# Kernel tuning notes

Measured on AMD Instinct MI355X. Metric: run time of the kernel, lower is better.

## Reference

```python
import jax, jax.numpy as jnp
import numpy as np

DIM = 1024
H = 16
HD = 64

def setup_inputs() -> dict:
    key = jax.random.key(0)
    ks = jax.random.split(key, 5)
    x = jax.random.normal(ks[0], (2, 2048, DIM), dtype=jnp.float32)
    gamma = jnp.ones((DIM,), jnp.float32)
    beta = jnp.zeros((DIM,), jnp.float32)
    w_qkv = jax.random.normal(ks[1], (DIM, 3 * H * HD), dtype=jnp.float32) * (DIM ** -0.5)
    w_out = jax.random.normal(ks[2], (H * HD, DIM), dtype=jnp.float32) * ((H * HD) ** -0.5)
    b_out = jnp.zeros((DIM,), jnp.float32)
    return {"x": x, "gamma": gamma, "beta": beta, "w_qkv": w_qkv, "w_out": w_out, "b_out": b_out}

def reference(x, gamma, beta, w_qkv, w_out, b_out):
    # LayerNorm (pre-norm)
    mu = jnp.mean(x, axis=-1, keepdims=True)
    var = jnp.var(x, axis=-1, keepdims=True)
    xn = (x - mu) * jax.lax.rsqrt(var + 1e-5) * gamma + beta
    # QKV projection (no bias)
    qkv = xn @ w_qkv  # (b, n, 3*h*hd)
    q, k, v = jnp.split(qkv, 3, axis=-1)
    b, n, _ = x.shape
    split = lambda t: t.reshape(b, n, H, HD).transpose(0, 2, 1, 3)  # b h n d
    q, k, v = split(q), split(k), split(v)
    scale = HD ** -0.5
    scores = jnp.einsum('bhqd,bhkd->bhqk', q, k) * scale
    weights = jax.nn.softmax(scores, axis=-1)
    attn = jnp.einsum('bhqk,bhkd->bhqd', weights, v)  # b h n d
    attn = attn.transpose(0, 2, 1, 3).reshape(b, n, H * HD)
    # output projection (dropout is identity in eval)
    return attn @ w_out + b_out
```

## Files before the change

### kernel.cpp

```cpp
#include <hip/hip_runtime.h>
#include <hip/hip_bf16.h>


typedef _Float16 f16x8 __attribute__((ext_vector_type(8)));
typedef _Float16 f16x4 __attribute__((ext_vector_type(4)));
typedef float    f32x4 __attribute__((ext_vector_type(4)));

#define DIM   1024
#define NH    16
#define HD2   64
#define SEQ   2048
#define ROWS  4096
#define QKVN  3072

__device__ __forceinline__ void async_copy16(void* lds, const void* gsrc) {
    __builtin_amdgcn_global_load_lds(
        (const __attribute__((address_space(1))) unsigned int*)gsrc,
        (__attribute__((address_space(3))) unsigned int*)lds, 16, 0, 0);
}

__global__ __launch_bounds__(256) void ln_kernel(
    const float* __restrict__ x, const float* __restrict__ gamma,
    const float* __restrict__ beta, _Float16* __restrict__ xn) {
    const int row = blockIdx.x;
    const int t = threadIdx.x;
    const float4 v = reinterpret_cast<const float4*>(x + (size_t)row * DIM)[t];
    float s1 = v.x + v.y + v.z + v.w;
    float s2 = v.x * v.x + v.y * v.y + v.z * v.z + v.w * v.w;
    for (int off = 32; off; off >>= 1) {
        s1 += __shfl_down(s1, off);
        s2 += __shfl_down(s2, off);
    }
    __shared__ float red[8];
    const int wv = t >> 6, lane = t & 63;
    if (lane == 0) { red[wv * 2] = s1; red[wv * 2 + 1] = s2; }
    __syncthreads();
    s1 = red[0] + red[2] + red[4] + red[6];
    s2 = red[1] + red[3] + red[5] + red[7];
    const float mu = s1 * (1.0f / DIM);
    const float var = s2 * (1.0f / DIM) - mu * mu;
    const float rstd = rsqrtf(var + 1e-5f);
    const float4 g = reinterpret_cast<const float4*>(gamma)[t];
    const float4 bb = reinterpret_cast<const float4*>(beta)[t];
    f16x4 o;
    o[0] = (_Float16)((v.x - mu) * rstd * g.x + bb.x);
    o[1] = (_Float16)((v.y - mu) * rstd * g.y + bb.y);
    o[2] = (_Float16)((v.z - mu) * rstd * g.z + bb.z);
    o[3] = (_Float16)((v.w - mu) * rstd * g.w + bb.w);
    reinterpret_cast<f16x4*>(xn + (size_t)row * DIM)[t] = o;
}

__global__ __launch_bounds__(256) void transpose_cvt_kernel(
    const float* __restrict__ in, _Float16* __restrict__ out, int R, int C) {
    __shared__ float tile[32][33];
    const int c0 = blockIdx.x * 32, r0 = blockIdx.y * 32;
    const int tx = threadIdx.x, ty = threadIdx.y;
#pragma unroll
    for (int i = 0; i < 4; i++)
        tile[ty + i * 8][tx] = in[(size_t)(r0 + ty + i * 8) * C + c0 + tx];
    __syncthreads();
#pragma unroll
    for (int i = 0; i < 4; i++)
        out[(size_t)(c0 + ty + i * 8) * R + r0 + tx] = (_Float16)tile[tx][ty + i * 8];
}

__global__ __launch_bounds__(256) void gemm_qkv_kernel(
    const _Float16* __restrict__ A, const _Float16* __restrict__ Bt,
    _Float16* __restrict__ qk, _Float16* __restrict__ vT, int K) {
    __shared__ _Float16 Al[2][128 * 32];
    __shared__ _Float16 Bl[2][128 * 32];
    const int t = threadIdx.x, wv = t >> 6, lane = t & 63;
    const int lg = lane >> 4, lr = lane & 15;
    const int wr = wv >> 1, wc = wv & 1;
    const int m0 = blockIdx.y * 128, n0 = blockIdx.x * 128;

    f32x4 acc[4][4] = {};

    const int srow = t >> 2, sk = (t & 3) * 8;
    const _Float16* Ag0 = A + (size_t)(m0 + srow) * K + sk;
    const _Float16* Bg0 = Bt + (size_t)(n0 + srow) * K + sk;

    auto STAGE = [&](int buf, int k0) {
        _Float16* Alw = &Al[buf][wv * 512];
        _Float16* Blw = &Bl[buf][wv * 512];
        async_copy16(Alw,        Ag0 + k0);
        async_copy16(Alw + 2048, Ag0 + (size_t)64 * K + k0);
        async_copy16(Blw,        Bg0 + k0);
        async_copy16(Blw + 2048, Bg0 + (size_t)64 * K + k0);
    };

    STAGE(0, 0);
    asm volatile("s_waitcnt vmcnt(0)" ::: "memory");
    __builtin_amdgcn_s_barrier();
    int cur = 0;
    for (int k0 = 0; k0 < K; k0 += 32) {
        if (k0 + 32 < K) STAGE(cur ^ 1, k0 + 32);
        const _Float16* Ab = &Al[cur][0];
        const _Float16* Bb = &Bl[cur][0];
        f16x8 af[4], bfr[4];
#pragma unroll
        for (int m = 0; m < 4; m++)
            af[m] = *reinterpret_cast<const f16x8*>(&Ab[(wr * 64 + m * 16 + lr) * 32 + lg * 8]);
#pragma unroll
        for (int n = 0; n < 4; n++)
            bfr[n] = *reinterpret_cast<const f16x8*>(&Bb[(wc * 64 + n * 16 + lr) * 32 + lg * 8]);
#pragma unroll
        for (int m = 0; m < 4; m++)
#pragma unroll
            for (int n = 0; n < 4; n++)
                acc[m][n] = __builtin_amdgcn_mfma_f32_16x16x32_f16(af[m], bfr[n], acc[m][n], 0, 0, 0);
        asm volatile("s_waitcnt vmcnt(0)" ::: "memory");
        __builtin_amdgcn_s_barrier();
        cur ^= 1;
    }

    if (n0 < 2 * DIM) {
#pragma unroll
        for (int m = 0; m < 4; m++) {
            const int row = m0 + wr * 64 + m * 16 + lg * 4;
#pragma unroll
            for (int n = 0; n < 4; n++) {
                const int col = n0 + wc * 64 + n * 16 + lr;
#pragma unroll
                for (int jj = 0; jj < 4; jj++)
                    qk[(size_t)(row + jj) * 2048 + col] = (_Float16)acc[m][n][jj];
            }
        }
    } else {
#pragma unroll
        for (int m = 0; m < 4; m++) {
            const int row = m0 + wr * 64 + m * 16 + lg * 4;
            const int b = row >> 11, nn = row & 2047;
#pragma unroll
            for (int n = 0; n < 4; n++) {
                const int vcol = n0 + wc * 64 + n * 16 + lr - 2 * DIM;
                f16x4 pk;
#pragma unroll
                for (int jj = 0; jj < 4; jj++) pk[jj] = (_Float16)acc[m][n][jj];
                *reinterpret_cast<f16x4*>(&vT[(size_t)(b * 1024 + vcol) * SEQ + nn]) = pk;
            }
        }
    }
}

__global__ __launch_bounds__(256) void gemm_out_kernel(
    const _Float16* __restrict__ A, const _Float16* __restrict__ Bt,
    float* __restrict__ C, const float* __restrict__ bias, int N, int K) {
    __shared__ _Float16 Al[2][128 * 32];
    __shared__ _Float16 Bl[2][64 * 32];
    const int t = threadIdx.x, wv = t >> 6, lane = t & 63;
    const int lg = lane >> 4, lr = lane & 15;
    const int wr = wv >> 1, wc = wv & 1;
    const int m0 = blockIdx.y * 128, n0 = blockIdx.x * 64;

    f32x4 acc[4][2] = {};

    const int srow = t >> 2, sk = (t & 3) * 8;
    const _Float16* Ag0 = A + (size_t)(m0 + srow) * K + sk;
    const _Float16* Bg0 = Bt + (size_t)(n0 + srow) * K + sk;

    auto STAGE = [&](int buf, int k0) {
        _Float16* Alw = &Al[buf][wv * 512];
        _Float16* Blw = &Bl[buf][wv * 512];
        async_copy16(Alw,        Ag0 + k0);
        async_copy16(Alw + 2048, Ag0 + (size_t)64 * K + k0);
        async_copy16(Blw,        Bg0 + k0);
    };

    STAGE(0, 0);
    asm volatile("s_waitcnt vmcnt(0)" ::: "memory");
    __builtin_amdgcn_s_barrier();
    int cur = 0;
    for (int k0 = 0; k0 < K; k0 += 32) {
        if (k0 + 32 < K) STAGE(cur ^ 1, k0 + 32);
        const _Float16* Ab = &Al[cur][0];
        const _Float16* Bb = &Bl[cur][0];
        f16x8 af[4], bfr[2];
#pragma unroll
        for (int m = 0; m < 4; m++)
            af[m] = *reinterpret_cast<const f16x8*>(&Ab[(wr * 64 + m * 16 + lr) * 32 + lg * 8]);
#pragma unroll
        for (int n = 0; n < 2; n++)
            bfr[n] = *reinterpret_cast<const f16x8*>(&Bb[(wc * 32 + n * 16 + lr) * 32 + lg * 8]);
#pragma unroll
        for (int m = 0; m < 4; m++)
#pragma unroll
            for (int n = 0; n < 2; n++)
                acc[m][n] = __builtin_amdgcn_mfma_f32_16x16x32_f16(af[m], bfr[n], acc[m][n], 0, 0, 0);
        asm volatile("s_waitcnt vmcnt(0)" ::: "memory");
        __builtin_amdgcn_s_barrier();
        cur ^= 1;
    }

#pragma unroll
    for (int m = 0; m < 4; m++) {
        const int row = m0 + wr * 64 + m * 16 + lg * 4;
#pragma unroll
        for (int n = 0; n < 2; n++) {
            const int col = n0 + wc * 32 + n * 16 + lr;
            const float bo = bias[col];
#pragma unroll
            for (int jj = 0; jj < 4; jj++)
                C[(size_t)(row + jj) * N + col] = acc[m][n][jj] + bo;
        }
    }
}

__global__ __launch_bounds__(256) void attn_fa_kernel(
    const _Float16* __restrict__ qk, const _Float16* __restrict__ vT,
    _Float16* __restrict__ attn) {
    const int id = blockIdx.x;
    const int nid = (id & 7) * 128 + (id >> 3);
    const int bh = nid >> 5, b = bh >> 4, h = bh & 15;
    const int q0 = (nid & 31) * 64;
    const int t = threadIdx.x, wv = t >> 6, lane = t & 63;
    const int lg = lane >> 4, lr = lane & 15;

    __shared__ _Float16 Kl[64][72];
    __shared__ _Float16 Vt[64][72];
    __shared__ _Float16 PT[4][16][72];

    const size_t qrow = (size_t)(b * SEQ + q0 + wv * 16 + lr);
    const _Float16* qp = qk + qrow * 2048 + h * HD2;
    f16x8 qf0 = *reinterpret_cast<const f16x8*>(qp + lg * 8);
    f16x8 qf1 = *reinterpret_cast<const f16x8*>(qp + 32 + lg * 8);
    qf0 = qf0 * (_Float16)0.125f;
    qf1 = qf1 * (_Float16)0.125f;

    f32x4 o[4] = {};
    float mrun = -INFINITY, lrun = 0.f;

    const int sr = t >> 3, sc = (t & 7) * 8;
    const _Float16* kbase = qk + (size_t)(b * SEQ + sr) * 2048 + DIM + h * HD2 + sc;
    const _Float16* vbase = vT + (size_t)(bh * HD2 + sr) * SEQ + sc;

    f16x8 rk0 = *reinterpret_cast<const f16x8*>(kbase);
    f16x8 rk1 = *reinterpret_cast<const f16x8*>(kbase + (size_t)32 * 2048);
    f16x8 rv0 = *reinterpret_cast<const f16x8*>(vbase);
    f16x8 rv1 = *reinterpret_cast<const f16x8*>(vbase + (size_t)32 * SEQ);

    for (int kv0 = 0; kv0 < SEQ; kv0 += 64) {
        __builtin_amdgcn_s_barrier();
        *reinterpret_cast<f16x8*>(&Kl[sr][sc])      = rk0;
        *reinterpret_cast<f16x8*>(&Kl[sr + 32][sc]) = rk1;
        *reinterpret_cast<f16x8*>(&Vt[sr][sc])      = rv0;
        *reinterpret_cast<f16x8*>(&Vt[sr + 32][sc]) = rv1;
        if (kv0 + 64 < SEQ) {
            const _Float16* kp = kbase + (size_t)(kv0 + 64) * 2048;
            const _Float16* vp = vbase + (kv0 + 64);
            rk0 = *reinterpret_cast<const f16x8*>(kp);
            rk1 = *reinterpret_cast<const f16x8*>(kp + (size_t)32 * 2048);
            rv0 = *reinterpret_cast<const f16x8*>(vp);
            rv1 = *reinterpret_cast<const f16x8*>(vp + (size_t)32 * SEQ);
        }
        asm volatile("s_waitcnt lgkmcnt(0)" ::: "memory");
        __builtin_amdgcn_s_barrier();

        f32x4 s[4];
#pragma unroll
        for (int n = 0; n < 4; n++) {
            f16x8 kf0 = *reinterpret_cast<const f16x8*>(&Kl[n * 16 + lr][lg * 8]);
            f16x8 kf1 = *reinterpret_cast<const f16x8*>(&Kl[n * 16 + lr][32 + lg * 8]);
            f32x4 z = {0.f, 0.f, 0.f, 0.f};
            __builtin_amdgcn_s_setprio(1);
            z = __builtin_amdgcn_mfma_f32_16x16x32_f16(kf0, qf0, z, 0, 0, 0);
            z = __builtin_amdgcn_mfma_f32_16x16x32_f16(kf1, qf1, z, 0, 0, 0);
            __builtin_amdgcn_s_setprio(0);
            s[n] = z;
        }

        float m1 = fmaxf(fmaxf(s[0][0], s[0][1]), fmaxf(s[0][2], s[0][3]));
#pragma unroll
        for (int n = 1; n < 4; n++)
            m1 = fmaxf(m1, fmaxf(fmaxf(s[n][0], s[n][1]), fmaxf(s[n][2], s[n][3])));
        m1 = fmaxf(m1, __shfl_xor(m1, 16));
        m1 = fmaxf(m1, __shfl_xor(m1, 32));
        if (!__all(m1 - mrun <= 8.f)) {
            const float mnew = fmaxf(mrun, m1);
            const float corr = __expf(mrun - mnew);
            mrun = mnew;
            lrun *= corr;
#pragma unroll
            for (int dn = 0; dn < 4; dn++) o[dn] *= corr;
        }
        float rsum = 0.f;
#pragma unroll
        for (int n = 0; n < 4; n++)
#pragma unroll
            for (int jj = 0; jj < 4; jj++) {
                const float p = __expf(s[n][jj] - mrun);
                s[n][jj] = p;
                rsum += p;
            }
        rsum += __shfl_xor(rsum, 16);
        rsum += __shfl_xor(rsum, 32);
        lrun += rsum;

#pragma unroll
        for (int n = 0; n < 4; n++) {
            f16x4 pk;
#pragma unroll
            for (int jj = 0; jj < 4; jj++) pk[jj] = (_Float16)s[n][jj];
            *reinterpret_cast<f16x4*>(&PT[wv][lr][n * 16 + lg * 4]) = pk;
        }
        f16x8 pa0 = *reinterpret_cast<const f16x8*>(&PT[wv][lr][lg * 8]);
        f16x8 pa1 = *reinterpret_cast<const f16x8*>(&PT[wv][lr][32 + lg * 8]);

#pragma unroll
        for (int dn = 0; dn < 4; dn++) {
            f16x8 vf0 = *reinterpret_cast<const f16x8*>(&Vt[dn * 16 + lr][lg * 8]);
            f16x8 vf1 = *reinterpret_cast<const f16x8*>(&Vt[dn * 16 + lr][32 + lg * 8]);
            __builtin_amdgcn_s_setprio(1);
            o[dn] = __builtin_amdgcn_mfma_f32_16x16x32_f16(vf0, pa0, o[dn], 0, 0, 0);
            o[dn] = __builtin_amdgcn_mfma_f32_16x16x32_f16(vf1, pa1, o[dn], 0, 0, 0);
            __builtin_amdgcn_s_setprio(0);
        }
    }

    const float inv = 1.0f / lrun;
    const size_t orow = (size_t)(b * SEQ + q0 + wv * 16 + lr);
#pragma unroll
    for (int dn = 0; dn < 4; dn++) {
        f16x4 pk;
#pragma unroll
        for (int jj = 0; jj < 4; jj++) pk[jj] = (_Float16)(o[dn][jj] * inv);
        *reinterpret_cast<f16x4*>(&attn[orow * DIM + h * HD2 + dn * 16 + lg * 4]) = pk;
    }
}

extern "C" void kernel_launch(void* const* d_in, const int* in_sizes, int n_in,
                              void* d_out, int out_size, void* d_ws, size_t ws_size,
                              hipStream_t stream) {
    const float* x     = (const float*)d_in[0];
    const float* gamma = (const float*)d_in[1];
    const float* beta  = (const float*)d_in[2];
    const float* w_qkv = (const float*)d_in[3];
    const float* w_out = (const float*)d_in[4];
    const float* b_out = (const float*)d_in[5];
    float* out = (float*)d_out;

    _Float16* ws    = (_Float16*)d_ws;
    _Float16* xn    = ws;
    _Float16* wqkvT = xn + (size_t)ROWS * DIM;
    _Float16* woutT = wqkvT + (size_t)QKVN * DIM;
    _Float16* qk    = woutT + (size_t)DIM * DIM;
    _Float16* vT    = qk + (size_t)ROWS * 2048;
    _Float16* attnb = xn;

    ln_kernel<<<ROWS, 256, 0, stream>>>(x, gamma, beta, xn);
    transpose_cvt_kernel<<<dim3(QKVN / 32, DIM / 32), dim3(32, 8), 0, stream>>>(w_qkv, wqkvT, DIM, QKVN);
    transpose_cvt_kernel<<<dim3(DIM / 32, DIM / 32), dim3(32, 8), 0, stream>>>(w_out, woutT, DIM, DIM);
    gemm_qkv_kernel<<<dim3(QKVN / 128, ROWS / 128), 256, 0, stream>>>(xn, wqkvT, qk, vT, DIM);
    attn_fa_kernel<<<1024, 256, 0, stream>>>(qk, vT, attnb);
    gemm_out_kernel<<<dim3(DIM / 64, ROWS / 128), 256, 0, stream>>>(attnb, woutT, out, b_out, DIM, DIM);
}
```

Measured before the change: 217.2 us.

## Load K/V fragments directly from global memory, dropping LDS staging and barriers

The attention kernel no longer stages K and V tiles in shared memory with register prefetch and block barriers. Each wave now reads its MFMA operand fragments for K and V straight from global memory every iteration. This removes the LDS writes, LDS reads and two barriers per tile. In exchange, the four waves in a block each fetch the same K/V data (4x redundant global/L2 traffic), and the software prefetch is lost, so load latency sits exposed right before the MFMAs.

```diff
diff --git a/kernel.cpp b/kernel.cpp
--- a/kernel.cpp
+++ b/kernel.cpp
@@ -216,8 +216,6 @@
     const int t = threadIdx.x, wv = t >> 6, lane = t & 63;
     const int lg = lane >> 4, lr = lane & 15;
 
-    __shared__ _Float16 Kl[64][72];
-    __shared__ _Float16 Vt[64][72];
     __shared__ _Float16 PT[4][16][72];
 
     const size_t qrow = (size_t)(b * SEQ + q0 + wv * 16 + lr);
@@ -230,41 +228,31 @@
     f32x4 o[4] = {};
     float mrun = -INFINITY, lrun = 0.f;
 
-    const int sr = t >> 3, sc = (t & 7) * 8;
-    const _Float16* kbase = qk + (size_t)(b * SEQ + sr) * 2048 + DIM + h * HD2 + sc;
-    const _Float16* vbase = vT + (size_t)(bh * HD2 + sr) * SEQ + sc;
-
-    f16x8 rk0 = *reinterpret_cast<const f16x8*>(kbase);
-    f16x8 rk1 = *reinterpret_cast<const f16x8*>(kbase + (size_t)32 * 2048);
-    f16x8 rv0 = *reinterpret_cast<const f16x8*>(vbase);
-    f16x8 rv1 = *reinterpret_cast<const f16x8*>(vbase + (size_t)32 * SEQ);
+    const _Float16* kp = qk + (size_t)(b * SEQ + lr) * 2048 + DIM + h * HD2 + lg * 8;
+    const _Float16* vp = vT + (size_t)(bh * HD2 + lr) * SEQ + lg * 8;
 
     for (int kv0 = 0; kv0 < SEQ; kv0 += 64) {
-        __builtin_amdgcn_s_barrier();
-        *reinterpret_cast<f16x8*>(&Kl[sr][sc])      = rk0;
-        *reinterpret_cast<f16x8*>(&Kl[sr + 32][sc]) = rk1;
-        *reinterpret_cast<f16x8*>(&Vt[sr][sc])      = rv0;
-        *reinterpret_cast<f16x8*>(&Vt[sr + 32][sc]) = rv1;
-        if (kv0 + 64 < SEQ) {
-            const _Float16* kp = kbase + (size_t)(kv0 + 64) * 2048;
-            const _Float16* vp = vbase + (kv0 + 64);
-            rk0 = *reinterpret_cast<const f16x8*>(kp);
-            rk1 = *reinterpret_cast<const f16x8*>(kp + (size_t)32 * 2048);
-            rv0 = *reinterpret_cast<const f16x8*>(vp);
-            rv1 = *reinterpret_cast<const f16x8*>(vp + (size_t)32 * SEQ);
-        }
-        asm volatile("s_waitcnt lgkmcnt(0)" ::: "memory");
-        __builtin_amdgcn_s_barrier();
+        f16x8 kf0[4], kf1[4], vf0[4], vf1[4];
+#pragma unroll
+        for (int n = 0; n < 4; n++) {
+            const _Float16* kpn = kp + (size_t)(kv0 + n * 16) * 2048;
+            kf0[n] = *reinterpret_cast<const f16x8*>(kpn);
+            kf1[n] = *reinterpret_cast<const f16x8*>(kpn + 32);
+        }
+#pragma unroll
+        for (int dn = 0; dn < 4; dn++) {
+            const _Float16* vpn = vp + (size_t)dn * 16 * SEQ + kv0;
+            vf0[dn] = *reinterpret_cast<const f16x8*>(vpn);
+            vf1[dn] = *reinterpret_cast<const f16x8*>(vpn + 32);
+        }
 
         f32x4 s[4];
 #pragma unroll
         for (int n = 0; n < 4; n++) {
-            f16x8 kf0 = *reinterpret_cast<const f16x8*>(&Kl[n * 16 + lr][lg * 8]);
-            f16x8 kf1 = *reinterpret_cast<const f16x8*>(&Kl[n * 16 + lr][32 + lg * 8]);
             f32x4 z = {0.f, 0.f, 0.f, 0.f};
             __builtin_amdgcn_s_setprio(1);
-            z = __builtin_amdgcn_mfma_f32_16x16x32_f16(kf0, qf0, z, 0, 0, 0);
-            z = __builtin_amdgcn_mfma_f32_16x16x32_f16(kf1, qf1, z, 0, 0, 0);
+            z = __builtin_amdgcn_mfma_f32_16x16x32_f16(kf0[n], qf0, z, 0, 0, 0);
+            z = __builtin_amdgcn_mfma_f32_16x16x32_f16(kf1[n], qf1, z, 0, 0, 0);
             __builtin_amdgcn_s_setprio(0);
             s[n] = z;
         }
@@ -308,11 +296,9 @@
 
 #pragma unroll
         for (int dn = 0; dn < 4; dn++) {
-            f16x8 vf0 = *reinterpret_cast<const f16x8*>(&Vt[dn * 16 + lr][lg * 8]);
-            f16x8 vf1 = *reinterpret_cast<const f16x8*>(&Vt[dn * 16 + lr][32 + lg * 8]);
             __builtin_amdgcn_s_setprio(1);
-            o[dn] = __builtin_amdgcn_mfma_f32_16x16x32_f16(vf0, pa0, o[dn], 0, 0, 0);
-            o[dn] = __builtin_amdgcn_mfma_f32_16x16x32_f16(vf1, pa1, o[dn], 0, 0, 0);
+            o[dn] = __builtin_amdgcn_mfma_f32_16x16x32_f16(vf0[dn], pa0, o[dn], 0, 0, 0);
+            o[dn] = __builtin_amdgcn_mfma_f32_16x16x32_f16(vf1[dn], pa1, o[dn], 0, 0, 0);
             __builtin_amdgcn_s_setprio(0);
         }
     }
```

Result: slower. 370.2 us (+70.4%).

## Triple-buffer GEMM K-loop prefetch and merge LN/transpose into one prologue kernel

Applied to the files above, without the earlier changes.

Both GEMM kernels move from double-buffered LDS staging with a full vmcnt(0) wait each iteration to a three-stage ring. Two tiles are kept in flight and only the oldest is waited on (vmcnt(4)/vmcnt(3)), so global loads overlap more of the MFMA work. The LayerNorm and the two weight transpose/convert kernels are fused into a single launch that dispatches on block index, removing two kernel launches. The cost is more LDS per block (48KB for the QKV GEMM), which may reduce occupancy.

```diff
diff --git a/kernel.cpp b/kernel.cpp
--- a/kernel.cpp
+++ b/kernel.cpp
@@ -12,6 +12,7 @@
 #define SEQ   2048
 #define ROWS  4096
 #define QKVN  3072
+#define NT    32
 
 __device__ __forceinline__ void async_copy16(void* lds, const void* gsrc) {
     __builtin_amdgcn_global_load_lds(
@@ -19,42 +20,57 @@
         (__attribute__((address_space(3))) unsigned int*)lds, 16, 0, 0);
 }
 
-__global__ __launch_bounds__(256) void ln_kernel(
+__global__ __launch_bounds__(256) void prologue_kernel(
     const float* __restrict__ x, const float* __restrict__ gamma,
-    const float* __restrict__ beta, _Float16* __restrict__ xn) {
-    const int row = blockIdx.x;
+    const float* __restrict__ beta, _Float16* __restrict__ xn,
+    const float* __restrict__ w_qkv, _Float16* __restrict__ wqkvT,
+    const float* __restrict__ w_out, _Float16* __restrict__ woutT) {
+    __shared__ float smem[32 * 33];
+    const int bid = blockIdx.x;
     const int t = threadIdx.x;
-    const float4 v = reinterpret_cast<const float4*>(x + (size_t)row * DIM)[t];
-    float s1 = v.x + v.y + v.z + v.w;
-    float s2 = v.x * v.x + v.y * v.y + v.z * v.z + v.w * v.w;
-    for (int off = 32; off; off >>= 1) {
-        s1 += __shfl_down(s1, off);
-        s2 += __shfl_down(s2, off);
-    }
-    __shared__ float red[8];
-    const int wv = t >> 6, lane = t & 63;
-    if (lane == 0) { red[wv * 2] = s1; red[wv * 2 + 1] = s2; }
-    __syncthreads();
-    s1 = red[0] + red[2] + red[4] + red[6];
-    s2 = red[1] + red[3] + red[5] + red[7];
-    const float mu = s1 * (1.0f / DIM);
-    const float var = s2 * (1.0f / DIM) - mu * mu;
-    const float rstd = rsqrtf(var + 1e-5f);
-    const float4 g = reinterpret_cast<const float4*>(gamma)[t];
-    const float4 bb = reinterpret_cast<const float4*>(beta)[t];
-    f16x4 o;
-    o[0] = (_Float16)((v.x - mu) * rstd * g.x + bb.x);
-    o[1] = (_Float16)((v.y - mu) * rstd * g.y + bb.y);
-    o[2] = (_Float16)((v.z - mu) * rstd * g.z + bb.z);
-    o[3] = (_Float16)((v.w - mu) * rstd * g.w + bb.w);
-    reinterpret_cast<f16x4*>(xn + (size_t)row * DIM)[t] = o;
-}
-
-__global__ __launch_bounds__(256) void transpose_cvt_kernel(
-    const float* __restrict__ in, _Float16* __restrict__ out, int R, int C) {
-    __shared__ float tile[32][33];
-    const int c0 = blockIdx.x * 32, r0 = blockIdx.y * 32;
-    const int tx = threadIdx.x, ty = threadIdx.y;
+    if (bid < ROWS) {
+        const int row = bid;
+        const float4 v = reinterpret_cast<const float4*>(x + (size_t)row * DIM)[t];
+        float s1 = v.x + v.y + v.z + v.w;
+        float s2 = v.x * v.x + v.y * v.y + v.z * v.z + v.w * v.w;
+        for (int off = 32; off; off >>= 1) {
+            s1 += __shfl_down(s1, off);
+            s2 += __shfl_down(s2, off);
+        }
+        const int wv = t >> 6, lane = t & 63;
+        if (lane == 0) { smem[wv * 2] = s1; smem[wv * 2 + 1] = s2; }
+        __syncthreads();
+        s1 = smem[0] + smem[2] + smem[4] + smem[6];
+        s2 = smem[1] + smem[3] + smem[5] + smem[7];
+        const float mu = s1 * (1.0f / DIM);
+        const float var = s2 * (1.0f / DIM) - mu * mu;
+        const float rstd = rsqrtf(var + 1e-5f);
+        const float4 g = reinterpret_cast<const float4*>(gamma)[t];
+        const float4 bb = reinterpret_cast<const float4*>(beta)[t];
+        f16x4 o;
+        o[0] = (_Float16)((v.x - mu) * rstd * g.x + bb.x);
+        o[1] = (_Float16)((v.y - mu) * rstd * g.y + bb.y);
+        o[2] = (_Float16)((v.z - mu) * rstd * g.z + bb.z);
+        o[3] = (_Float16)((v.w - mu) * rstd * g.w + bb.w);
+        reinterpret_cast<f16x4*>(xn + (size_t)row * DIM)[t] = o;
+        return;
+    }
+    const float* in;
+    _Float16* out;
+    int C, bx, by;
+    if (bid < ROWS + (QKVN / 32) * (DIM / 32)) {
+        const int q = bid - ROWS;
+        in = w_qkv; out = wqkvT; C = QKVN;
+        bx = q % (QKVN / 32); by = q / (QKVN / 32);
+    } else {
+        const int q = bid - ROWS - (QKVN / 32) * (DIM / 32);
+        in = w_out; out = woutT; C = DIM;
+        bx = q % (DIM / 32); by = q / (DIM / 32);
+    }
+    const int R = DIM;
+    const int c0 = bx * 32, r0 = by * 32;
+    const int tx = t & 31, ty = t >> 5;
+    float (*tile)[33] = reinterpret_cast<float(*)[33]>(smem);
 #pragma unroll
     for (int i = 0; i < 4; i++)
         tile[ty + i * 8][tx] = in[(size_t)(r0 + ty + i * 8) * C + c0 + tx];
@@ -66,9 +82,10 @@
 
 __global__ __launch_bounds__(256) void gemm_qkv_kernel(
     const _Float16* __restrict__ A, const _Float16* __restrict__ Bt,
-    _Float16* __restrict__ qk, _Float16* __restrict__ vT, int K) {
-    __shared__ _Float16 Al[2][128 * 32];
-    __shared__ _Float16 Bl[2][128 * 32];
+    _Float16* __restrict__ qk, _Float16* __restrict__ vT) {
+    const int K = DIM;
+    __shared__ _Float16 Al[3][128 * 32];
+    __shared__ _Float16 Bl[3][128 * 32];
     const int t = threadIdx.x, wv = t >> 6, lane = t & 63;
     const int lg = lane >> 4, lr = lane & 15;
     const int wr = wv >> 1, wc = wv & 1;
@@ -90,11 +107,16 @@
     };
 
     STAGE(0, 0);
-    asm volatile("s_waitcnt vmcnt(0)" ::: "memory");
-    __builtin_amdgcn_s_barrier();
+    STAGE(1, 32);
     int cur = 0;
-    for (int k0 = 0; k0 < K; k0 += 32) {
-        if (k0 + 32 < K) STAGE(cur ^ 1, k0 + 32);
+    for (int tt = 0; tt < NT; ++tt) {
+        if (tt < NT - 1) asm volatile("s_waitcnt vmcnt(4)" ::: "memory");
+        else             asm volatile("s_waitcnt vmcnt(0)" ::: "memory");
+        __builtin_amdgcn_s_barrier();
+        if (tt + 2 < NT) {
+            const int wb = cur >= 1 ? cur - 1 : 2;
+            STAGE(wb, (tt + 2) * 32);
+        }
         const _Float16* Ab = &Al[cur][0];
         const _Float16* Bb = &Bl[cur][0];
         f16x8 af[4], bfr[4];
@@ -109,9 +131,8 @@
 #pragma unroll
             for (int n = 0; n < 4; n++)
                 acc[m][n] = __builtin_amdgcn_mfma_f32_16x16x32_f16(af[m], bfr[n], acc[m][n], 0, 0, 0);
-        asm volatile("s_waitcnt vmcnt(0)" ::: "memory");
-        __builtin_amdgcn_s_barrier();
-        cur ^= 1;
+        asm volatile("s_waitcnt lgkmcnt(0)" ::: "memory");
+        cur = cur < 2 ? cur + 1 : 0;
     }
 
     if (n0 < 2 * DIM) {
@@ -145,9 +166,10 @@
 
 __global__ __launch_bounds__(256) void gemm_out_kernel(
     const _Float16* __restrict__ A, const _Float16* __restrict__ Bt,
-    float* __restrict__ C, const float* __restrict__ bias, int N, int K) {
-    __shared__ _Float16 Al[2][128 * 32];
-    __shared__ _Float16 Bl[2][64 * 32];
+    float* __restrict__ C, const float* __restrict__ bias) {
+    const int K = DIM, N = DIM;
+    __shared__ _Float16 Al[3][128 * 32];
+    __shared__ _Float16 Bl[3][64 * 32];
     const int t = threadIdx.x, wv = t >> 6, lane = t & 63;
     const int lg = lane >> 4, lr = lane & 15;
     const int wr = wv >> 1, wc = wv & 1;
@@ -168,11 +190,16 @@
     };
 
     STAGE(0, 0);
-    asm volatile("s_waitcnt vmcnt(0)" ::: "memory");
-    __builtin_amdgcn_s_barrier();
+    STAGE(1, 32);
     int cur = 0;
-    for (int k0 = 0; k0 < K; k0 += 32) {
-        if (k0 + 32 < K) STAGE(cur ^ 1, k0 + 32);
+    for (int tt = 0; tt < NT; ++tt) {
+        if (tt < NT - 1) asm volatile("s_waitcnt vmcnt(3)" ::: "memory");
+        else             asm volatile("s_waitcnt vmcnt(0)" ::: "memory");
+        __builtin_amdgcn_s_barrier();
+        if (tt + 2 < NT) {
+            const int wb = cur >= 1 ? cur - 1 : 2;
+            STAGE(wb, (tt + 2) * 32);
+        }
         const _Float16* Ab = &Al[cur][0];
         const _Float16* Bb = &Bl[cur][0];
         f16x8 af[4], bfr[2];
@@ -187,9 +214,8 @@
 #pragma unroll
             for (int n = 0; n < 2; n++)
                 acc[m][n] = __builtin_amdgcn_mfma_f32_16x16x32_f16(af[m], bfr[n], acc[m][n], 0, 0, 0);
-        asm volatile("s_waitcnt vmcnt(0)" ::: "memory");
-        __builtin_amdgcn_s_barrier();
-        cur ^= 1;
+        asm volatile("s_waitcnt lgkmcnt(0)" ::: "memory");
+        cur = cur < 2 ? cur + 1 : 0;
     }
 
 #pragma unroll
@@ -347,10 +373,9 @@
     _Float16* vT    = qk + (size_t)ROWS * 2048;
     _Float16* attnb = xn;
 
-    ln_kernel<<<ROWS, 256, 0, stream>>>(x, gamma, beta, xn);
-    transpose_cvt_kernel<<<dim3(QKVN / 32, DIM / 32), dim3(32, 8), 0, stream>>>(w_qkv, wqkvT, DIM, QKVN);
-    transpose_cvt_kernel<<<dim3(DIM / 32, DIM / 32), dim3(32, 8), 0, stream>>>(w_out, woutT, DIM, DIM);
-    gemm_qkv_kernel<<<dim3(QKVN / 128, ROWS / 128), 256, 0, stream>>>(xn, wqkvT, qk, vT, DIM);
+    const int pro_blocks = ROWS + (QKVN / 32) * (DIM / 32) + (DIM / 32) * (DIM / 32);
+    prologue_kernel<<<pro_blocks, 256, 0, stream>>>(x, gamma, beta, xn, w_qkv, wqkvT, w_out, woutT);
+    gemm_qkv_kernel<<<dim3(QKVN / 128, ROWS / 128), 256, 0, stream>>>(xn, wqkvT, qk, vT);
     attn_fa_kernel<<<1024, 256, 0, stream>>>(qk, vT, attnb);
-    gemm_out_kernel<<<dim3(DIM / 64, ROWS / 128), 256, 0, stream>>>(attnb, woutT, out, b_out, DIM, DIM);
-}
+    gemm_out_kernel<<<dim3(DIM / 64, ROWS / 128), 256, 0, stream>>>(attnb, woutT, out, b_out);
+}
```

After: 220.7 us. No clear change (+1.6%).
